# Kernel optimization log

Measured on AMD Instinct MI355X. Metric: run time of the kernel, lower is better.

The kernel has to match this reference:

```python
import jax, jax.numpy as jnp
import numpy as np

D_E = 128
D_R = 128  # must equal D_E for the original torch code to typecheck
BN_EPS = 1e-5


def setup_inputs() -> dict:
    key = jax.random.key(0)
    ks = jax.random.split(key, 8)
    B, S = 16, 2048
    h = jax.random.normal(ks[0], (B, S, D_E), dtype=jnp.float32)
    r = jax.random.normal(ks[1], (B, S, D_R), dtype=jnp.float32)
    t = jax.random.normal(ks[2], (B, S, D_E), dtype=jnp.float32)
    # Xavier-uniform core tensor W: (d_r, d_e, d_e)
    limit = float(np.sqrt(6.0 / (D_R + D_E * D_E)))
    W = jax.random.uniform(ks[3], (D_R, D_E, D_E), minval=-limit, maxval=limit, dtype=jnp.float32)
    # BatchNorm1d params/buffers (inference mode)
    gamma0 = jnp.ones((D_E,), jnp.float32)
    beta0 = jnp.zeros((D_E,), jnp.float32)
    mean0 = 0.1 * jax.random.normal(ks[4], (D_E,), dtype=jnp.float32)
    var0 = jnp.abs(1.0 + 0.1 * jax.random.normal(ks[5], (D_E,), dtype=jnp.float32))
    gamma1 = jnp.ones((D_E,), jnp.float32)
    beta1 = jnp.zeros((D_E,), jnp.float32)
    mean1 = 0.1 * jax.random.normal(ks[6], (D_E,), dtype=jnp.float32)
    var1 = jnp.abs(1.0 + 0.1 * jax.random.normal(ks[7], (D_E,), dtype=jnp.float32))
    return {"h": h, "r": r, "t": t, "W": W,
            "gamma0": gamma0, "beta0": beta0, "mean0": mean0, "var0": var0,
            "gamma1": gamma1, "beta1": beta1, "mean1": mean1, "var1": var1}


def reference(h, r, t, W, gamma0, beta0, mean0, var0, gamma1, beta1, mean1, var1):
    B, S, D = h.shape  # D == d_e == d_r
    N = B * S
    # BatchNorm1d in eval mode over last dim; dropout is identity in eval.
    h_bn = (h - mean0) * jax.lax.rsqrt(var0 + BN_EPS) * gamma0 + beta0
    t_bn = (t - mean1) * jax.lax.rsqrt(var1 + BN_EPS) * gamma1 + beta1
    r2 = r.reshape(N, D)
    # torch.matmul((N,d_r), (d_r,d_e,d_e)) broadcasts -> shape (d_r, N, d_e):
    #   out[k, n, j] = sum_i r2[n, i] * W[k, i, j]
    # followed by .view(N, d_e, d_e) which reinterprets the flat buffer.
    W_mat = jnp.einsum('ni,kij->knj', r2, W).reshape(N, D, D)  # (N, d_e, d_e) after scrambled view
    # hr[n, j] = sum_d h_bn[n, d] * W_mat[n, d, j]
    hr = jnp.einsum('nd,ndj->nj', h_bn.reshape(N, D), W_mat)
    scores = jnp.sum(hr * t_bn.reshape(N, D), axis=-1)  # (N,)
    return scores.reshape(B, S)
```

## Files before the change

### kernel.cpp

```cpp
#include <hip/hip_runtime.h>


typedef __attribute__((ext_vector_type(8))) short bf16x8;
typedef __attribute__((ext_vector_type(4))) float f32x4;

#define BN_EPS 1e-5f

__device__ inline unsigned short f2bf(float f) {
  unsigned u = __builtin_bit_cast(unsigned, f);
  u += 0x7FFFu + ((u >> 16) & 1u);
  return (unsigned short)(u >> 16);
}
__device__ inline unsigned pack2bf(float lo, float hi) {
  return (unsigned)f2bf(lo) | ((unsigned)f2bf(hi) << 16);
}
__device__ inline bf16x8 cvt8(f32x4 lo, f32x4 hi) {
  bf16x8 o;
  o[0] = (short)f2bf(lo[0]); o[1] = (short)f2bf(lo[1]);
  o[2] = (short)f2bf(lo[2]); o[3] = (short)f2bf(lo[3]);
  o[4] = (short)f2bf(hi[0]); o[5] = (short)f2bf(hi[1]);
  o[6] = (short)f2bf(hi[2]); o[7] = (short)f2bf(hi[3]);
  return o;
}

__device__ inline int xcd_map(int bid) { return (bid & 7) * 64 + (bid >> 3); }

__global__ __launch_bounds__(256) void k_vA(
    const float* __restrict__ t, const float* __restrict__ W,
    const float* __restrict__ gamma1, const float* __restrict__ beta1,
    const float* __restrict__ mean1, const float* __restrict__ var1,
    unsigned short* __restrict__ V) {
  const int tid = threadIdx.x;
  const int wv_ = tid >> 6;
  const int lane = tid & 63;
  const int l16 = lane & 15;
  const int quad = lane >> 4;

  const int w = xcd_map(blockIdx.x) * 4 + wv_;
  const int k = w >> 4;
  const int rg = w & 15;
  const int nrow = k * 256 + rg * 16 + l16;

  const float* tp = t + (size_t)nrow * 128;
  bf16x8 tf[4];
#pragma unroll
  for (int ks = 0; ks < 4; ++ks) {
    const int K0 = ks * 32 + quad * 8;
    f32x4 g0 = *(const f32x4*)(gamma1 + K0), g1 = *(const f32x4*)(gamma1 + K0 + 4);
    f32x4 b0 = *(const f32x4*)(beta1  + K0), b1 = *(const f32x4*)(beta1  + K0 + 4);
    f32x4 m0 = *(const f32x4*)(mean1  + K0), m1 = *(const f32x4*)(mean1  + K0 + 4);
    f32x4 v0 = *(const f32x4*)(var1   + K0), v1 = *(const f32x4*)(var1   + K0 + 4);
    f32x4 t0 = *(const f32x4*)(tp + K0),     t1 = *(const f32x4*)(tp + K0 + 4);
    f32x4 lo, hi;
    for (int q = 0; q < 4; ++q) {
      const float s0 = g0[q] * rsqrtf(v0[q] + BN_EPS);
      lo[q] = t0[q] * s0 + (b0[q] - m0[q] * s0);
      const float s1 = g1[q] * rsqrtf(v1[q] + BN_EPS);
      hi[q] = t1[q] * s1 + (b1[q] - m1[q] * s1);
    }
    tf[ks] = cvt8(lo, hi);
  }

  const float* wp = W + (size_t)k * 16384 + (size_t)l16 * 128;

  f32x4 acc[8];
#pragma unroll
  for (int nt = 0; nt < 8; ++nt) acc[nt] = (f32x4){0.f, 0.f, 0.f, 0.f};

#pragma unroll
  for (int ks = 0; ks < 4; ++ks) {
    const int K0 = ks * 32 + quad * 8;
#pragma unroll
    for (int nt = 0; nt < 8; ++nt) {
      f32x4 w0 = *(const f32x4*)(wp + nt * 2048 + K0);
      f32x4 w1 = *(const f32x4*)(wp + nt * 2048 + K0 + 4);
      acc[nt] = __builtin_amdgcn_mfma_f32_16x16x32_bf16(cvt8(w0, w1), tf[ks],
                                                        acc[nt], 0, 0, 0);
    }
  }

  const size_t np = (size_t)nrow * 128;
#pragma unroll
  for (int nt = 0; nt < 8; ++nt) {
    unsigned two[2];
    two[0] = pack2bf(acc[nt][0], acc[nt][1]);
    two[1] = pack2bf(acc[nt][2], acc[nt][3]);
    *(uint2*)(V + np + nt * 16 + quad * 4) = *(uint2*)two;
  }
}

__global__ __launch_bounds__(256) void k_B2(
    const float* __restrict__ h, const float* __restrict__ r,
    const float* __restrict__ gamma0, const float* __restrict__ beta0,
    const float* __restrict__ mean0, const float* __restrict__ var0,
    const unsigned short* __restrict__ V, float* __restrict__ out) {
  const int tid = threadIdx.x;
  const int wv_ = tid >> 6;
  const int lane = tid & 63;
  const int l16 = lane & 15;
  const int quad = lane >> 4;

  const int w = xcd_map(blockIdx.x) * 4 + wv_;
  const int low = w >> 3;
  const int kg = w & 7;
  const int kk = kg * 16 + l16;
  const size_t nprow = (size_t)kk * 256 + low;

  const unsigned short* vp = V + nprow * 128;
  bf16x8 vf[4];
#pragma unroll
  for (int ks = 0; ks < 4; ++ks)
    vf[ks] = *(const bf16x8*)(vp + ks * 32 + quad * 8);

  const float* rp = r + ((size_t)low * 128 + l16) * 128;

  f32x4 acc[8];
#pragma unroll
  for (int nt = 0; nt < 8; ++nt) acc[nt] = (f32x4){0.f, 0.f, 0.f, 0.f};

#pragma unroll
  for (int ks = 0; ks < 4; ++ks) {
    const int K0 = ks * 32 + quad * 8;
#pragma unroll
    for (int nt = 0; nt < 8; ++nt) {
      f32x4 r0 = *(const f32x4*)(rp + nt * 2048 + K0);
      f32x4 r1 = *(const f32x4*)(rp + nt * 2048 + K0 + 4);
      acc[nt] = __builtin_amdgcn_mfma_f32_16x16x32_bf16(cvt8(r0, r1), vf[ks],
                                                        acc[nt], 0, 0, 0);
    }
  }

  const float* hp = h + nprow * 128;
  float s = 0.f;
#pragma unroll
  for (int nt = 0; nt < 8; ++nt) {
    const int a0 = nt * 16 + quad * 4;
    f32x4 hv = *(const f32x4*)(hp + a0);
    f32x4 g  = *(const f32x4*)(gamma0 + a0);
    f32x4 be = *(const f32x4*)(beta0  + a0);
    f32x4 mu = *(const f32x4*)(mean0  + a0);
    f32x4 va = *(const f32x4*)(var0   + a0);
    for (int q = 0; q < 4; ++q) {
      const float sc = g[q] * rsqrtf(va[q] + BN_EPS);
      const float hb = hv[q] * sc + (be[q] - mu[q] * sc);
      s += hb * acc[nt][q];
    }
  }
  s += __shfl_xor(s, 16, 64);
  s += __shfl_xor(s, 32, 64);
  if (quad == 0) out[nprow] = s;
}

extern "C" void kernel_launch(void* const* d_in, const int* in_sizes, int n_in,
                              void* d_out, int out_size, void* d_ws, size_t ws_size,
                              hipStream_t stream) {
  const float* h      = (const float*)d_in[0];
  const float* r      = (const float*)d_in[1];
  const float* t      = (const float*)d_in[2];
  const float* W      = (const float*)d_in[3];
  const float* gamma0 = (const float*)d_in[4];
  const float* beta0  = (const float*)d_in[5];
  const float* mean0  = (const float*)d_in[6];
  const float* var0   = (const float*)d_in[7];
  const float* gamma1 = (const float*)d_in[8];
  const float* beta1  = (const float*)d_in[9];
  const float* mean1  = (const float*)d_in[10];
  const float* var1   = (const float*)d_in[11];
  float* out = (float*)d_out;

  unsigned short* V = (unsigned short*)d_ws;

  k_vA<<<512, 256, 0, stream>>>(t, W, gamma1, beta1, mean1, var1, V);
  k_B2<<<512, 256, 0, stream>>>(h, r, gamma0, beta0, mean0, var0, V, out);
}
```

Measured before the change: 138.1 us.

## Stage W and r tiles in LDS as bf16 shared across waves

```diff
diff --git a/kernel.cpp b/kernel.cpp
--- a/kernel.cpp
+++ b/kernel.cpp
@@ -2,14 +2,20 @@
 
 
 typedef __attribute__((ext_vector_type(8))) short bf16x8;
+typedef __attribute__((ext_vector_type(4))) short s16x4;
 typedef __attribute__((ext_vector_type(4))) float f32x4;
 
+#define DPAD 136
 #define BN_EPS 1e-5f
 
 __device__ inline unsigned short f2bf(float f) {
   unsigned u = __builtin_bit_cast(unsigned, f);
   u += 0x7FFFu + ((u >> 16) & 1u);
   return (unsigned short)(u >> 16);
+}
+__device__ inline float bf2f(unsigned short h) {
+  unsigned u = ((unsigned)h) << 16;
+  return __builtin_bit_cast(float, u);
 }
 __device__ inline unsigned pack2bf(float lo, float hi) {
   return (unsigned)f2bf(lo) | ((unsigned)f2bf(hi) << 16);
@@ -25,21 +31,24 @@
 
 __device__ inline int xcd_map(int bid) { return (bid & 7) * 64 + (bid >> 3); }
 
-__global__ __launch_bounds__(256) void k_vA(
+__global__ __launch_bounds__(256, 3) void k_A(
     const float* __restrict__ t, const float* __restrict__ W,
     const float* __restrict__ gamma1, const float* __restrict__ beta1,
     const float* __restrict__ mean1, const float* __restrict__ var1,
     unsigned short* __restrict__ V) {
+  __shared__ short LW[128 * DPAD];
   const int tid = threadIdx.x;
+  const int c = tid & 31;
+  const int rr = tid >> 5;
   const int wv_ = tid >> 6;
   const int lane = tid & 63;
   const int l16 = lane & 15;
   const int quad = lane >> 4;
 
-  const int w = xcd_map(blockIdx.x) * 4 + wv_;
-  const int k = w >> 4;
-  const int rg = w & 15;
-  const int nrow = k * 256 + rg * 16 + l16;
+  const int wg = xcd_map(blockIdx.x);
+  const int k = wg >> 2;
+  const int quarter = wg & 3;
+  const int nrow = k * 256 + quarter * 64 + wv_ * 16 + l16;
 
   const float* tp = t + (size_t)nrow * 128;
   bf16x8 tf[4];
@@ -61,23 +70,34 @@
     tf[ks] = cvt8(lo, hi);
   }
 
-  const float* wp = W + (size_t)k * 16384 + (size_t)l16 * 128;
+  const float* wbase = W + (size_t)k * 16384;
+#pragma unroll
+  for (int it = 0; it < 16; ++it) {
+    const int m = it * 8 + rr;
+    f32x4 wvv = *(const f32x4*)(wbase + m * 128 + c * 4);
+    s16x4 wb;
+    for (int q = 0; q < 4; ++q) wb[q] = (short)f2bf(wvv[q]);
+    *(s16x4*)(&LW[m * DPAD + c * 4]) = wb;
+  }
+  __syncthreads();
 
   f32x4 acc[8];
 #pragma unroll
   for (int nt = 0; nt < 8; ++nt) acc[nt] = (f32x4){0.f, 0.f, 0.f, 0.f};
 
+  __builtin_amdgcn_s_setprio(1);
 #pragma unroll
   for (int ks = 0; ks < 4; ++ks) {
     const int K0 = ks * 32 + quad * 8;
-#pragma unroll
-    for (int nt = 0; nt < 8; ++nt) {
-      f32x4 w0 = *(const f32x4*)(wp + nt * 2048 + K0);
-      f32x4 w1 = *(const f32x4*)(wp + nt * 2048 + K0 + 4);
-      acc[nt] = __builtin_amdgcn_mfma_f32_16x16x32_bf16(cvt8(w0, w1), tf[ks],
-                                                        acc[nt], 0, 0, 0);
-    }
-  }
+    bf16x8 b[8];
+#pragma unroll
+    for (int nt = 0; nt < 8; ++nt)
+      b[nt] = *(const bf16x8*)(&LW[(nt * 16 + l16) * DPAD + K0]);
+#pragma unroll
+    for (int nt = 0; nt < 8; ++nt)
+      acc[nt] = __builtin_amdgcn_mfma_f32_16x16x32_bf16(b[nt], tf[ks], acc[nt], 0, 0, 0);
+  }
+  __builtin_amdgcn_s_setprio(0);
 
   const size_t np = (size_t)nrow * 128;
 #pragma unroll
@@ -89,21 +109,24 @@
   }
 }
 
-__global__ __launch_bounds__(256) void k_B2(
+__global__ __launch_bounds__(256, 3) void k_B(
     const float* __restrict__ h, const float* __restrict__ r,
     const float* __restrict__ gamma0, const float* __restrict__ beta0,
     const float* __restrict__ mean0, const float* __restrict__ var0,
     const unsigned short* __restrict__ V, float* __restrict__ out) {
+  __shared__ short LR[128 * DPAD];
   const int tid = threadIdx.x;
+  const int c = tid & 31;
+  const int rr = tid >> 5;
   const int wv_ = tid >> 6;
   const int lane = tid & 63;
   const int l16 = lane & 15;
   const int quad = lane >> 4;
 
-  const int w = xcd_map(blockIdx.x) * 4 + wv_;
-  const int low = w >> 3;
-  const int kg = w & 7;
-  const int kk = kg * 16 + l16;
+  const int wg = xcd_map(blockIdx.x);
+  const int low = wg >> 1;
+  const int half = wg & 1;
+  const int kk = half * 64 + wv_ * 16 + l16;
   const size_t nprow = (size_t)kk * 256 + low;
 
   const unsigned short* vp = V + nprow * 128;
@@ -112,23 +135,34 @@
   for (int ks = 0; ks < 4; ++ks)
     vf[ks] = *(const bf16x8*)(vp + ks * 32 + quad * 8);
 
-  const float* rp = r + ((size_t)low * 128 + l16) * 128;
+  const float* rbase = r + (size_t)low * 16384;
+#pragma unroll
+  for (int it = 0; it < 16; ++it) {
+    const int m = it * 8 + rr;
+    f32x4 rv = *(const f32x4*)(rbase + m * 128 + c * 4);
+    s16x4 rb;
+    for (int q = 0; q < 4; ++q) rb[q] = (short)f2bf(rv[q]);
+    *(s16x4*)(&LR[m * DPAD + c * 4]) = rb;
+  }
+  __syncthreads();
 
   f32x4 acc[8];
 #pragma unroll
   for (int nt = 0; nt < 8; ++nt) acc[nt] = (f32x4){0.f, 0.f, 0.f, 0.f};
 
+  __builtin_amdgcn_s_setprio(1);
 #pragma unroll
   for (int ks = 0; ks < 4; ++ks) {
     const int K0 = ks * 32 + quad * 8;
-#pragma unroll
-    for (int nt = 0; nt < 8; ++nt) {
-      f32x4 r0 = *(const f32x4*)(rp + nt * 2048 + K0);
-      f32x4 r1 = *(const f32x4*)(rp + nt * 2048 + K0 + 4);
-      acc[nt] = __builtin_amdgcn_mfma_f32_16x16x32_bf16(cvt8(r0, r1), vf[ks],
-                                                        acc[nt], 0, 0, 0);
-    }
-  }
+    bf16x8 b[8];
+#pragma unroll
+    for (int nt = 0; nt < 8; ++nt)
+      b[nt] = *(const bf16x8*)(&LR[(nt * 16 + l16) * DPAD + K0]);
+#pragma unroll
+    for (int nt = 0; nt < 8; ++nt)
+      acc[nt] = __builtin_amdgcn_mfma_f32_16x16x32_bf16(b[nt], vf[ks], acc[nt], 0, 0, 0);
+  }
+  __builtin_amdgcn_s_setprio(0);
 
   const float* hp = h + nprow * 128;
   float s = 0.f;
@@ -170,6 +204,6 @@
 
   unsigned short* V = (unsigned short*)d_ws;
 
-  k_vA<<<512, 256, 0, stream>>>(t, W, gamma1, beta1, mean1, var1, V);
-  k_B2<<<512, 256, 0, stream>>>(h, r, gamma0, beta0, mean0, var0, V, out);
-}
+  k_A<<<512, 256, 0, stream>>>(t, W, gamma1, beta1, mean1, var1, V);
+  k_B<<<512, 256, 0, stream>>>(h, r, gamma0, beta0, mean0, var0, V, out);
+}
```

After: 118.5 us. 14.2% less time.
